# Kernel tuning notes

Measured on AMD Instinct MI355X. Metric: run time of the kernel, lower is better.

## Reference

```python
import jax, jax.numpy as jnp
import numpy as np

HIDDEN_DIM = 64
VOCAB_SIZE = 128
NUM_SLOTS = 64
B, L = 256, 4096


def layer_norm(x, gamma, beta, eps=1e-5):
    mu = jnp.mean(x, axis=-1, keepdims=True)
    var = jnp.mean(jnp.square(x - mu), axis=-1, keepdims=True)
    return (x - mu) * jax.lax.rsqrt(var + eps) * gamma + beta


def _l2norm(x, axis=-1, eps=1e-12):
    # matches torch F.normalize: x / max(||x||, eps)
    n = jnp.sqrt(jnp.sum(jnp.square(x), axis=axis, keepdims=True))
    return x / jnp.maximum(n, eps)


def setup_inputs() -> dict:
    key = jax.random.key(0)
    ks = jax.random.split(key, 13)
    H, V, S = HIDDEN_DIM, VOCAB_SIZE, NUM_SLOTS
    return {
        "seq": jax.random.randint(ks[0], (B, L), 0, V),
        "embed_w": jax.random.normal(ks[1], (V, H), dtype=jnp.float32),
        # linear weights stored [in, out] (transposed vs torch)
        "w1": jax.random.normal(ks[2], (H, 2 * H), dtype=jnp.float32) * 0.05,
        "b1": jnp.zeros((2 * H,), dtype=jnp.float32),
        "w2": jax.random.normal(ks[3], (2 * H, H), dtype=jnp.float32) * 0.05,
        "b2": jnp.zeros((H,), dtype=jnp.float32),
        "ln_g": jnp.ones((H,), dtype=jnp.float32),
        "ln_b": jnp.zeros((H,), dtype=jnp.float32),
        "slot_keys": jax.random.normal(ks[4], (S, H), dtype=jnp.float32) * 0.1,
        "slot_vals": jax.random.normal(ks[5], (S, H), dtype=jnp.float32) * 0.1,
        "gate_w": jax.random.normal(ks[6], (H, S), dtype=jnp.float32) * 0.05,
        "gate_b": jnp.zeros((S,), dtype=jnp.float32),
        "out_w": jax.random.normal(ks[7], (H, V), dtype=jnp.float32) * 0.05,
        "out_b": jnp.zeros((V,), dtype=jnp.float32),
    }


def reference(seq, embed_w, w1, b1, w2, b2, ln_g, ln_b,
              slot_keys, slot_vals, gate_w, gate_b, out_w, out_b):
    h = embed_w[seq]                                   # [B, L, H]
    ff = jnp.maximum(h @ w1 + b1, 0.0) @ w2 + b2       # [B, L, H]
    h = layer_norm(h + ff, ln_g, ln_b)

    hw = h[:, :-1, :]                                  # written tokens [B, L-1, H]
    w = jax.nn.softmax(hw @ gate_w + gate_b, axis=-1)  # [B, L-1, S]
    # the per-step increment w_t (outer) h_t is independent of prior keys,
    # so the sequential loop collapses exactly to one contraction:
    keys = slot_keys[None, :, :] + jnp.einsum('btn,bth->bnh', w, hw)  # [B, S, H]
    vals = keys  # loop sets vals = keys every step; L > 1 here

    q = h[:, -1, :]                                    # [B, H]
    sim = jnp.einsum('bnh,bh->bn', _l2norm(keys), _l2norm(q))
    attn = jax.nn.softmax(sim, axis=-1)                # [B, S]
    ctx = jnp.einsum('bn,bnh->bh', attn, vals)         # [B, H]
    return ctx @ out_w + out_b                         # [B, V]
```

## Files before the change

kernel.cpp:

```cpp
#include <hip/hip_runtime.h>

#define HD 64
#define VC 128
#define NS 64
#define NB 256
#define SL 4096

__device__ __forceinline__ float wsum(float x) {
#pragma unroll
  for (int o = 32; o > 0; o >>= 1) x += __shfl_xor(x, o, 64);
  return x;
}
__device__ __forceinline__ float wmax(float x) {
#pragma unroll
  for (int o = 32; o > 0; o >>= 1) x = fmaxf(x, __shfl_xor(x, o, 64));
  return x;
}

__global__ __launch_bounds__(128) void build_tables(
    const float* __restrict__ embed, const float* __restrict__ w1, const float* __restrict__ b1,
    const float* __restrict__ w2, const float* __restrict__ b2,
    const float* __restrict__ ln_g, const float* __restrict__ ln_b,
    const float* __restrict__ gate_w, const float* __restrict__ gate_b,
    float* __restrict__ HN, float* __restrict__ WSM)
{
  const int v = blockIdx.x, t = threadIdx.x;
  __shared__ float s_e[HD], s_f1[2 * HD], s_hn[HD];

  if (t < HD) s_e[t] = embed[v * HD + t];
  __syncthreads();

  float acc = b1[t];
#pragma unroll 8
  for (int h = 0; h < HD; ++h)
    acc = fmaf(s_e[h], w1[h * 2 * HD + t], acc);
  s_f1[t] = fmaxf(acc, 0.f);
  __syncthreads();

  if (t < HD) {
    float a2 = b2[t];
#pragma unroll 8
    for (int j = 0; j < 2 * HD; ++j)
      a2 = fmaf(s_f1[j], w2[j * HD + t], a2);
    float x = s_e[t] + a2;
    float mu = wsum(x) * (1.f / 64.f);
    float d = x - mu;
    float var = wsum(d * d) * (1.f / 64.f);
    float hn = d * rsqrtf(var + 1e-5f) * ln_g[t] + ln_b[t];
    s_hn[t] = hn;
    HN[v * HD + t] = hn;
  }
  __syncthreads();

  if (t < NS) {
    float g = gate_b[t];
#pragma unroll 8
    for (int h = 0; h < HD; ++h)
      g = fmaf(s_hn[h], gate_w[h * NS + t], g);
    float m = wmax(g);
    float e = expf(g - m);
    float s = wsum(e);
    WSM[v * NS + t] = e / s;
  }
}

__global__ __launch_bounds__(1024) void batch_kernel(
    const int* __restrict__ seq, const float* __restrict__ HN, const float* __restrict__ WSM,
    const float* __restrict__ slot_keys, const float* __restrict__ out_w,
    const float* __restrict__ out_b, float* __restrict__ out)
{
  const int b = blockIdx.x, t = threadIdx.x;
  const int lane = t & 63, wave = t >> 6;

  __shared__ int s_cnt[VC];
  __shared__ int s_qtok;
  __align__(16) __shared__ float s_hn[VC * HD];
  __align__(16) __shared__ float s_wsm[VC * NS];
  __align__(16) __shared__ float s_keys[NS * HD];
  __align__(16) __shared__ float s_part[16 * HD];
  __shared__ float s_q[HD], s_sim[NS], s_attn[NS], s_ctx[HD];

  if (t < VC) s_cnt[t] = 0;
  __syncthreads();

  const int* sb = seq + b * SL;
  const int4 sv = ((const int4*)sb)[t];
  const float4 h0v = ((const float4*)HN)[t];
  const float4 h1v = ((const float4*)HN)[t + 1024];
  const float4 g0v = ((const float4*)WSM)[t];
  const float4 g1v = ((const float4*)WSM)[t + 1024];
  atomicAdd(&s_cnt[sv.x], 1);
  atomicAdd(&s_cnt[sv.y], 1);
  atomicAdd(&s_cnt[sv.z], 1);
  if (t != 1023) atomicAdd(&s_cnt[sv.w], 1);
  else s_qtok = sv.w;
  ((float4*)s_hn)[t] = h0v;
  ((float4*)s_hn)[t + 1024] = h1v;
  ((float4*)s_wsm)[t] = g0v;
  ((float4*)s_wsm)[t + 1024] = g1v;
  __syncthreads();

  if (t < HD) s_q[t] = s_hn[s_qtok * HD + t];
  {
    float4 a = ((const float4*)s_wsm)[t];
    float4 c = ((const float4*)s_wsm)[t + 1024];
    const float c0 = (float)s_cnt[t >> 4];
    const float c1 = (float)s_cnt[(t + 1024) >> 4];
    a.x *= c0; a.y *= c0; a.z *= c0; a.w *= c0;
    c.x *= c1; c.y *= c1; c.z *= c1; c.w *= c1;
    ((float4*)s_wsm)[t] = a;
    ((float4*)s_wsm)[t + 1024] = c;
  }
  __syncthreads();

  const int qt = t >> 8;
  const int tid = t & 255;
  const int n0 = (tid >> 4) << 2;
  const int h0 = (tid & 15) << 2;
  const float* hb = s_hn + qt * 32 * HD;
  const float* wb = s_wsm + qt * 32 * NS;

  float accv[4][4];
  if (qt == 0) {
#pragma unroll
    for (int r = 0; r < 4; ++r) {
      const float4 sk = *(const float4*)&slot_keys[(n0 + r) * HD + h0];
      accv[r][0] = sk.x; accv[r][1] = sk.y; accv[r][2] = sk.z; accv[r][3] = sk.w;
    }
  } else {
#pragma unroll
    for (int r = 0; r < 4; ++r)
#pragma unroll
      for (int c = 0; c < 4; ++c) accv[r][c] = 0.f;
  }

#pragma unroll 4
  for (int v = 0; v < 32; ++v) {
    const float4 hv = *(const float4*)&hb[v * HD + h0];
    const float4 wv = *(const float4*)&wb[v * NS + n0];
    accv[0][0] = fmaf(wv.x, hv.x, accv[0][0]);
    accv[0][1] = fmaf(wv.x, hv.y, accv[0][1]);
    accv[0][2] = fmaf(wv.x, hv.z, accv[0][2]);
    accv[0][3] = fmaf(wv.x, hv.w, accv[0][3]);
    accv[1][0] = fmaf(wv.y, hv.x, accv[1][0]);
    accv[1][1] = fmaf(wv.y, hv.y, accv[1][1]);
    accv[1][2] = fmaf(wv.y, hv.z, accv[1][2]);
    accv[1][3] = fmaf(wv.y, hv.w, accv[1][3]);
    accv[2][0] = fmaf(wv.z, hv.x, accv[2][0]);
    accv[2][1] = fmaf(wv.z, hv.y, accv[2][1]);
    accv[2][2] = fmaf(wv.z, hv.z, accv[2][2]);
    accv[2][3] = fmaf(wv.z, hv.w, accv[2][3]);
    accv[3][0] = fmaf(wv.w, hv.x, accv[3][0]);
    accv[3][1] = fmaf(wv.w, hv.y, accv[3][1]);
    accv[3][2] = fmaf(wv.w, hv.z, accv[3][2]);
    accv[3][3] = fmaf(wv.w, hv.w, accv[3][3]);
  }
  __syncthreads();

  float* kA = s_hn;
  float* kB = s_hn + NS * HD;
  if (qt == 1) {
#pragma unroll
    for (int r = 0; r < 4; ++r) {
      float4 st; st.x = accv[r][0]; st.y = accv[r][1]; st.z = accv[r][2]; st.w = accv[r][3];
      *(float4*)&kA[(n0 + r) * HD + h0] = st;
    }
  } else if (qt == 3) {
#pragma unroll
    for (int r = 0; r < 4; ++r) {
      float4 st; st.x = accv[r][0]; st.y = accv[r][1]; st.z = accv[r][2]; st.w = accv[r][3];
      *(float4*)&kB[(n0 + r) * HD + h0] = st;
    }
  }
  __syncthreads();
  if (qt == 0) {
#pragma unroll
    for (int r = 0; r < 4; ++r) {
      float4 p = *(const float4*)&kA[(n0 + r) * HD + h0];
      p.x += accv[r][0]; p.y += accv[r][1]; p.z += accv[r][2]; p.w += accv[r][3];
      *(float4*)&kA[(n0 + r) * HD + h0] = p;
    }
  } else if (qt == 2) {
#pragma unroll
    for (int r = 0; r < 4; ++r) {
      float4 p = *(const float4*)&kB[(n0 + r) * HD + h0];
      p.x += accv[r][0]; p.y += accv[r][1]; p.z += accv[r][2]; p.w += accv[r][3];
      *(float4*)&kB[(n0 + r) * HD + h0] = p;
    }
  }
  __syncthreads();
  {
    float4 a = ((const float4*)kA)[t];
    const float4 c = ((const float4*)kB)[t];
    a.x += c.x; a.y += c.y; a.z += c.z; a.w += c.w;
    ((float4*)s_keys)[t] = a;
  }
  __syncthreads();

  const float qv = s_q[lane];
  const float qn = fmaxf(sqrtf(wsum(qv * qv)), 1e-12f);
#pragma unroll
  for (int r = 0; r < 4; ++r) {
    const int n = (wave << 2) + r;
    const float kv = s_keys[n * HD + lane];
    const float kk = wsum(kv * kv);
    const float kq = wsum(kv * qv);
    if (lane == 0) s_sim[n] = kq / (fmaxf(sqrtf(kk), 1e-12f) * qn);
  }
  __syncthreads();

  if (wave == 0) {
    float svv = s_sim[lane];
    float m = wmax(svv);
    float e = expf(svv - m);
    float ssum = wsum(e);
    s_attn[lane] = e / ssum;
  }
  __syncthreads();

  {
    float c = 0.f;
#pragma unroll
    for (int r = 0; r < 4; ++r) {
      const int n = (wave << 2) + r;
      c = fmaf(s_attn[n], s_keys[n * HD + lane], c);
    }
    s_part[wave * HD + lane] = c;
  }
  __syncthreads();
  if (wave == 0) {
    float c = 0.f;
#pragma unroll
    for (int w = 0; w < 16; ++w) c += s_part[w * HD + lane];
    s_ctx[lane] = c;
  }
  __syncthreads();

  if (t < VC) {
    float o = out_b[t];
#pragma unroll 8
    for (int h = 0; h < HD; ++h)
      o = fmaf(s_ctx[h], out_w[h * VC + t], o);
    out[b * VC + t] = o;
  }
}

extern "C" void kernel_launch(void* const* d_in, const int* in_sizes, int n_in,
                              void* d_out, int out_size, void* d_ws, size_t ws_size,
                              hipStream_t stream) {
  const int* seq         = (const int*)d_in[0];
  const float* embed_w   = (const float*)d_in[1];
  const float* w1        = (const float*)d_in[2];
  const float* b1        = (const float*)d_in[3];
  const float* w2        = (const float*)d_in[4];
  const float* b2        = (const float*)d_in[5];
  const float* ln_g      = (const float*)d_in[6];
  const float* ln_b      = (const float*)d_in[7];
  const float* slot_keys = (const float*)d_in[8];
  const float* gate_w    = (const float*)d_in[10];
  const float* gate_b    = (const float*)d_in[11];
  const float* out_w     = (const float*)d_in[12];
  const float* out_b     = (const float*)d_in[13];
  float* out = (float*)d_out;

  float* HN  = (float*)d_ws;
  float* WSM = HN + VC * HD;

  build_tables<<<VC, 128, 0, stream>>>(embed_w, w1, b1, w2, b2, ln_g, ln_b,
                                       gate_w, gate_b, HN, WSM);
  batch_kernel<<<NB, 1024, 0, stream>>>(seq, HN, WSM, slot_keys, out_w, out_b, out);
}
```

Before: 101.7 us.

## Split table-build matvecs across threads and trim batch-kernel barriers

The table-building kernel now spreads the w2 and gate matvecs over all 128 threads, with partial sums reduced through shared memory, and uses four independent accumulators to break FMA dependency chains. The batch kernel issues the slot_keys loads before the first barrier, scales the gate table straight from registers instead of a shared-memory round trip, and drops one barrier. It also fuses the attention softmax into the context step using wave shuffles, which removes a second barrier and the s_attn array. The final reductions and the output matvec use multiple accumulators, which changes floating-point summation order slightly.

After: 93.64 us. 1.09x faster.

```diff
diff --git a/kernel.cpp b/kernel.cpp
--- a/kernel.cpp
+++ b/kernel.cpp
@@ -25,24 +25,41 @@
     float* __restrict__ HN, float* __restrict__ WSM)
 {
   const int v = blockIdx.x, t = threadIdx.x;
-  __shared__ float s_e[HD], s_f1[2 * HD], s_hn[HD];
+  __shared__ float s_e[HD], s_f1[2 * HD], s_hn[HD], s_red[128];
 
   if (t < HD) s_e[t] = embed[v * HD + t];
   __syncthreads();
 
-  float acc = b1[t];
-#pragma unroll 8
-  for (int h = 0; h < HD; ++h)
-    acc = fmaf(s_e[h], w1[h * 2 * HD + t], acc);
-  s_f1[t] = fmaxf(acc, 0.f);
+  {
+    float a0 = 0.f, a1 = 0.f, a2 = 0.f, a3 = 0.f;
+#pragma unroll
+    for (int h = 0; h < HD; h += 4) {
+      a0 = fmaf(s_e[h + 0], w1[(h + 0) * 2 * HD + t], a0);
+      a1 = fmaf(s_e[h + 1], w1[(h + 1) * 2 * HD + t], a1);
+      a2 = fmaf(s_e[h + 2], w1[(h + 2) * 2 * HD + t], a2);
+      a3 = fmaf(s_e[h + 3], w1[(h + 3) * 2 * HD + t], a3);
+    }
+    s_f1[t] = fmaxf(b1[t] + ((a0 + a1) + (a2 + a3)), 0.f);
+  }
+  __syncthreads();
+
+  {
+    const int col = t & 63;
+    const int j0 = (t >> 6) << 6;
+    float a0 = 0.f, a1 = 0.f, a2 = 0.f, a3 = 0.f;
+#pragma unroll
+    for (int j = 0; j < 64; j += 4) {
+      a0 = fmaf(s_f1[j0 + j + 0], w2[(j0 + j + 0) * HD + col], a0);
+      a1 = fmaf(s_f1[j0 + j + 1], w2[(j0 + j + 1) * HD + col], a1);
+      a2 = fmaf(s_f1[j0 + j + 2], w2[(j0 + j + 2) * HD + col], a2);
+      a3 = fmaf(s_f1[j0 + j + 3], w2[(j0 + j + 3) * HD + col], a3);
+    }
+    s_red[t] = (a0 + a1) + (a2 + a3);
+  }
   __syncthreads();
 
   if (t < HD) {
-    float a2 = b2[t];
-#pragma unroll 8
-    for (int j = 0; j < 2 * HD; ++j)
-      a2 = fmaf(s_f1[j], w2[j * HD + t], a2);
-    float x = s_e[t] + a2;
+    float x = s_e[t] + b2[t] + s_red[t] + s_red[t + 64];
     float mu = wsum(x) * (1.f / 64.f);
     float d = x - mu;
     float var = wsum(d * d) * (1.f / 64.f);
@@ -52,11 +69,23 @@
   }
   __syncthreads();
 
+  {
+    const int col = t & 63;
+    const int hh0 = (t >> 6) << 5;
+    float a0 = 0.f, a1 = 0.f, a2 = 0.f, a3 = 0.f;
+#pragma unroll
+    for (int h = 0; h < 32; h += 4) {
+      a0 = fmaf(s_hn[hh0 + h + 0], gate_w[(hh0 + h + 0) * NS + col], a0);
+      a1 = fmaf(s_hn[hh0 + h + 1], gate_w[(hh0 + h + 1) * NS + col], a1);
+      a2 = fmaf(s_hn[hh0 + h + 2], gate_w[(hh0 + h + 2) * NS + col], a2);
+      a3 = fmaf(s_hn[hh0 + h + 3], gate_w[(hh0 + h + 3) * NS + col], a3);
+    }
+    s_red[t] = (a0 + a1) + (a2 + a3);
+  }
+  __syncthreads();
+
   if (t < NS) {
-    float g = gate_b[t];
-#pragma unroll 8
-    for (int h = 0; h < HD; ++h)
-      g = fmaf(s_hn[h], gate_w[h * NS + t], g);
+    float g = gate_b[t] + s_red[t] + s_red[t + 64];
     float m = wmax(g);
     float e = expf(g - m);
     float s = wsum(e);
@@ -78,7 +107,20 @@
   __align__(16) __shared__ float s_wsm[VC * NS];
   __align__(16) __shared__ float s_keys[NS * HD];
   __align__(16) __shared__ float s_part[16 * HD];
-  __shared__ float s_q[HD], s_sim[NS], s_attn[NS], s_ctx[HD];
+  __shared__ float s_q[HD], s_sim[NS], s_ctx[HD];
+
+  const int qt = t >> 8;
+  const int tid = t & 255;
+  const int n0 = (tid >> 4) << 2;
+  const int h0 = (tid & 15) << 2;
+
+  float4 sk0, sk1, sk2, sk3;
+  if (qt == 0) {
+    sk0 = *(const float4*)&slot_keys[(n0 + 0) * HD + h0];
+    sk1 = *(const float4*)&slot_keys[(n0 + 1) * HD + h0];
+    sk2 = *(const float4*)&slot_keys[(n0 + 2) * HD + h0];
+    sk3 = *(const float4*)&slot_keys[(n0 + 3) * HD + h0];
+  }
 
   if (t < VC) s_cnt[t] = 0;
   __syncthreads();
@@ -96,37 +138,29 @@
   else s_qtok = sv.w;
   ((float4*)s_hn)[t] = h0v;
   ((float4*)s_hn)[t + 1024] = h1v;
-  ((float4*)s_wsm)[t] = g0v;
-  ((float4*)s_wsm)[t + 1024] = g1v;
-  __syncthreads();
-
-  if (t < HD) s_q[t] = s_hn[s_qtok * HD + t];
-  {
-    float4 a = ((const float4*)s_wsm)[t];
-    float4 c = ((const float4*)s_wsm)[t + 1024];
+  __syncthreads();
+
+  {
     const float c0 = (float)s_cnt[t >> 4];
     const float c1 = (float)s_cnt[(t + 1024) >> 4];
+    float4 a = g0v, c = g1v;
     a.x *= c0; a.y *= c0; a.z *= c0; a.w *= c0;
     c.x *= c1; c.y *= c1; c.z *= c1; c.w *= c1;
     ((float4*)s_wsm)[t] = a;
     ((float4*)s_wsm)[t + 1024] = c;
   }
-  __syncthreads();
-
-  const int qt = t >> 8;
-  const int tid = t & 255;
-  const int n0 = (tid >> 4) << 2;
-  const int h0 = (tid & 15) << 2;
+  if (t < HD) s_q[t] = s_hn[s_qtok * HD + t];
+  __syncthreads();
+
   const float* hb = s_hn + qt * 32 * HD;
   const float* wb = s_wsm + qt * 32 * NS;
 
   float accv[4][4];
   if (qt == 0) {
-#pragma unroll
-    for (int r = 0; r < 4; ++r) {
-      const float4 sk = *(const float4*)&slot_keys[(n0 + r) * HD + h0];
-      accv[r][0] = sk.x; accv[r][1] = sk.y; accv[r][2] = sk.z; accv[r][3] = sk.w;
-    }
+    accv[0][0] = sk0.x; accv[0][1] = sk0.y; accv[0][2] = sk0.z; accv[0][3] = sk0.w;
+    accv[1][0] = sk1.x; accv[1][1] = sk1.y; accv[1][2] = sk1.z; accv[1][3] = sk1.w;
+    accv[2][0] = sk2.x; accv[2][1] = sk2.y; accv[2][2] = sk2.z; accv[2][3] = sk2.w;
+    accv[3][0] = sk3.x; accv[3][1] = sk3.y; accv[3][2] = sk3.z; accv[3][3] = sk3.w;
   } else {
 #pragma unroll
     for (int r = 0; r < 4; ++r)
@@ -209,39 +243,45 @@
   }
   __syncthreads();
 
+  {
+    const float svv = s_sim[lane];
+    const float m = wmax(svv);
+    const float e = expf(svv - m);
+    const float ssum = wsum(e);
+    const float attn_l = e / ssum;
+    float c = 0.f;
+#pragma unroll
+    for (int r = 0; r < 4; ++r) {
+      const int n = (wave << 2) + r;
+      const float an = __shfl(attn_l, n, 64);
+      c = fmaf(an, s_keys[n * HD + lane], c);
+    }
+    s_part[wave * HD + lane] = c;
+  }
+  __syncthreads();
   if (wave == 0) {
-    float svv = s_sim[lane];
-    float m = wmax(svv);
-    float e = expf(svv - m);
-    float ssum = wsum(e);
-    s_attn[lane] = e / ssum;
-  }
-  __syncthreads();
-
-  {
-    float c = 0.f;
-#pragma unroll
-    for (int r = 0; r < 4; ++r) {
-      const int n = (wave << 2) + r;
-      c = fmaf(s_attn[n], s_keys[n * HD + lane], c);
-    }
-    s_part[wave * HD + lane] = c;
-  }
-  __syncthreads();
-  if (wave == 0) {
-    float c = 0.f;
-#pragma unroll
-    for (int w = 0; w < 16; ++w) c += s_part[w * HD + lane];
-    s_ctx[lane] = c;
+    float c0 = 0.f, c1 = 0.f, c2 = 0.f, c3 = 0.f;
+#pragma unroll
+    for (int w = 0; w < 16; w += 4) {
+      c0 += s_part[(w + 0) * HD + lane];
+      c1 += s_part[(w + 1) * HD + lane];
+      c2 += s_part[(w + 2) * HD + lane];
+      c3 += s_part[(w + 3) * HD + lane];
+    }
+    s_ctx[lane] = (c0 + c1) + (c2 + c3);
   }
   __syncthreads();
 
   if (t < VC) {
-    float o = out_b[t];
-#pragma unroll 8
-    for (int h = 0; h < HD; ++h)
-      o = fmaf(s_ctx[h], out_w[h * VC + t], o);
-    out[b * VC + t] = o;
+    float o0 = 0.f, o1 = 0.f, o2 = 0.f, o3 = 0.f;
+#pragma unroll
+    for (int h = 0; h < HD; h += 4) {
+      o0 = fmaf(s_ctx[h + 0], out_w[(h + 0) * VC + t], o0);
+      o1 = fmaf(s_ctx[h + 1], out_w[(h + 1) * VC + t], o1);
+      o2 = fmaf(s_ctx[h + 2], out_w[(h + 2) * VC + t], o2);
+      o3 = fmaf(s_ctx[h + 3], out_w[(h + 3) * VC + t], o3);
+    }
+    out[b * VC + t] = out_b[t] + ((o0 + o1) + (o2 + o3));
   }
 }
 
```
